# Kernel tuning notes

Hardware: AMD Instinct MI355X
Metric: run time of the kernel (lower is better)

## Reference

```python
import jax, jax.numpy as jnp
import numpy as np

E, L, M, F, S, P = 4, 10, 512, 128, 1000, 10  # envs, labels, max_sample, features, sample_size, batch_len


def setup_inputs() -> dict:
    key = jax.random.key(0)
    k1, k2, k3 = jax.random.split(key, 3)
    data_len = jax.random.randint(k1, (E, L), M // 2, M + 1, dtype=jnp.int32)
    matrix = jax.random.normal(k2, (E, L, M, F), dtype=jnp.float32)
    # zero out padded samples beyond data_len (as shape_to_matrix does)
    pad_mask = jnp.arange(M)[None, None, :, None] < data_len[:, :, None, None]
    matrix = matrix * pad_mask
    params = jnp.eye(F, dtype=jnp.float32) + 0.01 * jax.random.normal(k3, (F, F), dtype=jnp.float32)
    is_train_env = jnp.array([True, True, False, False])
    return {"matrix": matrix, "params": params, "data_len": data_len, "is_train_env": is_train_env}


def reference(matrix, params, data_len, is_train_env):
    lenf = data_len.astype(matrix.dtype)  # [E,L], torch keeps this as float32
    # __init__ preprocessing: normalize by mean std over sample dim (detached in torch)
    std = jax.lax.stop_gradient(jnp.std(matrix, axis=2).mean())
    mat = matrix / std
    # Silverman-style bandwidth on the normalized matrix (detached in torch)
    bw = jax.lax.stop_gradient(1.06 * (M ** (-1.0 / 5.0)) * jnp.std(mat, axis=2).mean())
    offset = jnp.exp(-0.5 / bw ** 2)
    proj = jnp.einsum('elmf,fg->elmg', mat, params)  # [E,L,M,F]
    left = jax.lax.stop_gradient(proj.min())   # .item() in torch -> constant
    right = jax.lax.stop_gradient(proj.max())
    delta = (right - left) / S
    x_grid = jnp.linspace(left, right, S)
    divisor = jnp.sqrt(2.0 * jnp.pi) * bw

    def step(acc, points):  # points: [P] grid chunk
        d2 = (proj[..., None] - points) ** 2                     # [E,L,M,F,P]
        s = jnp.sum(offset ** d2, axis=2)                        # [E,L,F,P]
        # remove contribution of zero-padded samples, then normalize by true count
        corr = (M - lenf)[:, :, None] * (offset ** (points ** 2))[None, None, :]  # [E,L,P]
        r = (s - corr[:, :, None, :]) / lenf[:, :, None, None]   # [E,L,F,P]
        d = jnp.sum(jnp.abs(r[:, None] - r[None, :]), axis=-1)   # [E,E,L,F] pairwise L1 over grid chunk
        return acc + d, None

    store_dis, _ = jax.lax.scan(step, jnp.zeros((E, E, L, F), proj.dtype), x_grid.reshape(S // P, P))
    store_dis = store_dis / divisor  # [E,E,L,F]

    idx = jnp.arange(E)
    upper = idx[:, None] < idx[None, :]                                   # all env pairs i<j
    train_pair = upper & is_train_env[:, None] & is_train_env[None, :]    # train env pairs i<j
    half = store_dis * (delta / 2.0)
    neg = jnp.array(-jnp.inf, half.dtype)
    test_results = jnp.where(upper[:, :, None, None], half, neg).max(axis=(0, 1))        # [L,F]
    train_results = jnp.where(train_pair[:, :, None, None], half, neg).max(axis=(0, 1))  # [L,F]
    train_dis = train_results.max(axis=0).mean()
    test_dis = test_results.max(axis=0).mean()
    return train_results, test_results, train_dis, test_dis
```

## Files before the change

### kernel.cpp

```cpp
#include <hip/hip_runtime.h>
#include <cmath>

#define E_ 4
#define L_ 10
#define M_ 512
#define F_ 128
#define S_ 1000

typedef unsigned int u32;
typedef _Float16 f16;
typedef __attribute__((ext_vector_type(8))) _Float16 v8h;
typedef __attribute__((ext_vector_type(4))) float v4f;

__device__ __forceinline__ float fexp2(float a){
#if __has_builtin(__builtin_amdgcn_exp2f)
  return __builtin_amdgcn_exp2f(a);
#else
  return exp2f(a);
#endif
}


__global__ __launch_bounds__(256) void k_pre(const float* __restrict__ mat,
                       const float* __restrict__ par,
                       float* __restrict__ projT, float* __restrict__ wsf){
  __shared__ float sm[2048];
  int b = blockIdx.x, tid = threadIdx.x;
  if (b >= 1280){
    int el = b - 1280;
    int fq = (tid & 31) * 4, part = tid >> 5;
    const float* base = mat + ((size_t)el * M_ + part*64) * F_;
    float4 s  = make_float4(0.f,0.f,0.f,0.f);
    float4 s2 = make_float4(0.f,0.f,0.f,0.f);
    #pragma unroll 8
    for (int i = 0; i < 64; i++){
      float4 v = *(const float4*)&base[i*F_ + fq];
      s.x += v.x; s.y += v.y; s.z += v.z; s.w += v.w;
      s2.x += v.x*v.x; s2.y += v.y*v.y; s2.z += v.z*v.z; s2.w += v.w*v.w;
    }
    ((float4*)sm)[tid]       = s;
    ((float4*)sm)[256 + tid] = s2;
    __syncthreads();
    for (int g = 4; g >= 1; g >>= 1){
      if (part < g){
        float4 o  = ((float4*)sm)[tid + g*32];
        float4 o2 = ((float4*)sm)[256 + tid + g*32];
        s.x += o.x; s.y += o.y; s.z += o.z; s.w += o.w;
        s2.x += o2.x; s2.y += o2.y; s2.z += o2.z; s2.w += o2.w;
        ((float4*)sm)[tid] = s;
        ((float4*)sm)[256 + tid] = s2;
      }
      __syncthreads();
    }
    if (part == 0){
      *(float4*)&wsf[2576 + el*128 + fq] = s;
      *(float4*)&wsf[7696 + el*128 + fq] = s2;
    }
    return;
  }
  int el = b >> 5, mt = (b & 31) * 16;
  int lane = tid & 63, wave = tid >> 6;
  int q = (lane >> 4) & 3, m16 = lane & 15;
  const float* arow = mat + ((size_t)el * M_ + mt + m16) * F_;
  v4f acc0 = {0.f,0.f,0.f,0.f}, acc1 = {0.f,0.f,0.f,0.f};
  #pragma unroll
  for (int c = 0; c < 4; c++){
    float4 a0 = *(const float4*)&arow[c*32 + q*8];
    float4 a1 = *(const float4*)&arow[c*32 + q*8 + 4];
    v8h af, b0, b1;
    af[0]=(f16)a0.x; af[1]=(f16)a0.y; af[2]=(f16)a0.z; af[3]=(f16)a0.w;
    af[4]=(f16)a1.x; af[5]=(f16)a1.y; af[6]=(f16)a1.z; af[7]=(f16)a1.w;
    const float* pb = par + (c*32 + q*8)*F_ + wave*32 + m16;
    #pragma unroll
    for (int j = 0; j < 8; j++){
      b0[j] = (f16)pb[j*F_];
      b1[j] = (f16)pb[j*F_ + 16];
    }
    acc0 = __builtin_amdgcn_mfma_f32_16x16x32_f16(af, b0, acc0, 0, 0, 0);
    acc1 = __builtin_amdgcn_mfma_f32_16x16x32_f16(af, b1, acc1, 0, 0, 0);
  }
  *(float4*)(projT + ((size_t)el*F_ + wave*32      + m16)*M_ + mt + q*4)
      = make_float4(acc0[0], acc0[1], acc0[2], acc0[3]);
  *(float4*)(projT + ((size_t)el*F_ + wave*32 + 16 + m16)*M_ + mt + q*4)
      = make_float4(acc1[0], acc1[1], acc1[2], acc1[3]);
  float lmin =  3.4e38f, lmax = -3.4e38f;
  #pragma unroll
  for (int r = 0; r < 4; r++){
    lmin = fminf(lmin, fminf(acc0[r], acc1[r]));
    lmax = fmaxf(lmax, fmaxf(acc0[r], acc1[r]));
  }
  #pragma unroll
  for (int d = 32; d >= 1; d >>= 1){
    lmin = fminf(lmin, __shfl_xor(lmin, d, 64));
    lmax = fmaxf(lmax, __shfl_xor(lmax, d, 64));
  }
  if (lane == 0){ sm[wave] = lmin; sm[8+wave] = lmax; }
  __syncthreads();
  if (tid == 0){
    wsf[16   + b] = fminf(fminf(sm[0], sm[1]), fminf(sm[2], sm[3]));
    wsf[1296 + b] = fmaxf(fmaxf(sm[8], sm[9]), fmaxf(sm[10], sm[11]));
  }
}

__global__ __launch_bounds__(1024) void k_red(float* __restrict__ wsf,
                                              float divisor, float k2c){
  __shared__ float rmn[1024], rmx[1024], rs[1024];
  int tid = threadIdx.x;
  float mn = 3.4e38f, mx = -3.4e38f, s = 0.f;
  for (int i = tid; i < 1280; i += 1024){
    mn = fminf(mn, wsf[16   + i]);
    mx = fmaxf(mx, wsf[1296 + i]);
  }
  for (int i = tid; i < 5120; i += 1024){
    float a  = wsf[2576 + i];
    float a2 = wsf[7696 + i];
    float mean = a * (1.0f/512.0f);
    float var  = a2 * (1.0f/512.0f) - mean*mean;
    s += sqrtf(fmaxf(var, 0.0f));
  }
  rmn[tid] = mn; rmx[tid] = mx; rs[tid] = s;
  __syncthreads();
  for (int g = 512; g >= 1; g >>= 1){
    if (tid < g){
      rmn[tid] = fminf(rmn[tid], rmn[tid+g]);
      rmx[tid] = fmaxf(rmx[tid], rmx[tid+g]);
      rs[tid] += rs[tid+g];
    }
    __syncthreads();
  }
  float rstd   = 5120.0f / rs[0];
  float leftS  = rmn[0] * rstd;
  float rightS = rmx[0] * rstd;
  float stepFS = (rightS - leftS) * (1.0f/999.0f);
  if (tid == 0){
    float inv2 = 1.0f / (2.0f * stepFS);
    wsf[0] = rstd * inv2;
    wsf[1] = leftS * inv2;
    wsf[2] = stepFS;
    wsf[3] = leftS;
    wsf[8] = ((rightS - leftS) * (1.0f/1000.0f)) * 0.5f / divisor;
  }
  float sh = 2.0f * stepFS;
  if (tid < 152){
    float v = 0.f;
    if (tid >= 8){
      int pr = (tid >> 1) - 4;
      int u  = pr - 34;
      float d = (tid & 1) ? (float)(2*u-1) * sh : (float)(2*u) * sh;
      v = (pr < 69) ? fexp2(k2c*d*d) : 0.f;
    }
    wsf[16 + tid] = v;
  }
  if (tid >= 256 && tid < 512){
    int idx = tid - 256;
    float xc = fmaf((float)(idx - 1), 4.0f*stepFS, leftS);
    wsf[168 + idx] = fexp2(k2c * xc * xc);
  }
}

__global__ __launch_bounds__(256, 4) void k_kde(const float* __restrict__ projT,
                      const int* __restrict__ dlen, const float* __restrict__ wsf,
                      float* __restrict__ dpair){
  __shared__ __align__(16) float smem[4752];
  int b = blockIdx.x;
  int l = b >> 7, f = b & 127;
  int tid = threadIdx.x, wave = tid >> 6, lane = tid & 63;
  int e = wave;
  const float4* gp = (const float4*)(projT + (((size_t)e * L_ + l) * F_ + f) * M_);
  float4 g0 = gp[lane], g1 = gp[lane + 64];
  float posScale = wsf[0], posOff = wsf[1];
  float lenE = (float)dlen[e*L_ + l];
  for (int idx = tid; idx < 824; idx += 256)
    ((float4*)(smem + 1024))[idx] = make_float4(0.f,0.f,0.f,0.f);
  if (tid < 38)
    ((float4*)(smem + 4320))[tid] = ((const float4*)(wsf + 16))[tid];
  if (tid >= 64 && tid < 128)
    ((float4*)(smem + 4472))[tid - 64] = ((const float4*)(wsf + 168))[tid - 64];
  __syncthreads();
  {
    float* hf = smem + 1024 + e*824;
    float pv[8] = {g0.x,g0.y,g0.z,g0.w,g1.x,g1.y,g1.z,g1.w};
    #pragma unroll
    for (int i = 0; i < 8; i++){
      float pos = fmaf(pv[i], posScale, -posOff);
      float n = floorf(pos + 0.5f);
      float d = pos - n;
      float wm = 0.5f*(0.5f-d)*(0.5f-d);
      float wp = 0.5f*(0.5f+d)*(0.5f+d);
      float w0 = 0.75f - d*d;
      int b0 = (int)n + 71;
      int b1 = b0 + 1, b2 = b0 + 2;
      int W0 = b0 + ((b0>>3)<<1);
      int W1 = b1 + ((b1>>3)<<1);
      int W2 = b2 + ((b2>>3)<<1);
      atomicAdd(&hf[W0], wm);
      atomicAdd(&hf[W1], w0);
      atomicAdd(&hf[W2], wp);
    }
  }
  __syncthreads();
  float rlen = 1.0f / lenE;
  float padc = 512.0f - lenE;
  {
    const float2* sK2 = (const float2*)(smem + 4320);
    const float* hl = smem + 1024 + e*824 + 10*lane;
    float2 c0 = sK2[72], c1 = sK2[73], c2 = sK2[74], c3 = sK2[75];
    float a0=0.f, a1=0.f, a2=0.f, a3=0.f;
    #pragma unroll 3
    for (int g = 0; g < 9; g++){
      float2 Hb[8];
      #pragma unroll
      for (int j = 0; j < 8; j++){
        int i = g*8 + j + 1;
        Hb[j] = *(const float2*)&hl[2*i + 2*(i>>2)];
      }
      #pragma unroll
      for (int j = 0; j < 8; j++){
        int i = g*8 + j + 1;
        a0 = fmaf(Hb[j].x, c0.x, fmaf(Hb[j].y, c0.y, a0));
        a1 = fmaf(Hb[j].x, c1.x, fmaf(Hb[j].y, c1.y, a1));
        a2 = fmaf(Hb[j].x, c2.x, fmaf(Hb[j].y, c2.y, a2));
        a3 = fmaf(Hb[j].x, c3.x, fmaf(Hb[j].y, c3.y, a3));
        c3 = c2; c2 = c1; c1 = c0; c0 = sK2[72 - i];
      }
    }
    int o0 = 4*lane;
    float4 cr = *(const float4*)&smem[4472 + o0];
    float4 stv = make_float4((a0 - padc*cr.x)*rlen, (a1 - padc*cr.y)*rlen,
                             (a2 - padc*cr.z)*rlen, (a3 - padc*cr.w)*rlen);
    *(float4*)&smem[e*256 + o0] = stv;
  }
  __syncthreads();
  float ps[6] = {0,0,0,0,0,0};
  if (tid < 250){
    float x[4][4];
    #pragma unroll
    for (int ee=0; ee<4; ee++){
      const float* st = &smem[ee*256 + tid];
      x[ee][0]=st[0]; x[ee][1]=st[1]; x[ee][2]=st[2]; x[ee][3]=st[3];
    }
    #pragma unroll
    for (int k=0; k<4; k++){
      float u = (float)k * 0.25f;
      float um1 = u - 1.0f, um2 = u - 2.0f, up1 = u + 1.0f;
      float w0 = -u * um1 * um2 * (1.0f/6.0f);
      float w1 = up1 * um1 * um2 * 0.5f;
      float w2 = -u * up1 * um2 * 0.5f;
      float w3 = u * up1 * um1 * (1.0f/6.0f);
      float rr[4];
      #pragma unroll
      for (int ee=0; ee<4; ee++)
        rr[ee] = w0*x[ee][0] + w1*x[ee][1] + w2*x[ee][2] + w3*x[ee][3];
      ps[0] += fabsf(rr[0]-rr[1]);
      ps[1] += fabsf(rr[0]-rr[2]);
      ps[2] += fabsf(rr[0]-rr[3]);
      ps[3] += fabsf(rr[1]-rr[2]);
      ps[4] += fabsf(rr[1]-rr[3]);
      ps[5] += fabsf(rr[2]-rr[3]);
    }
  }
  #pragma unroll
  for (int pr=0; pr<6; pr++){
    float v = ps[pr];
    #pragma unroll
    for (int d=32; d>=1; d>>=1) v += __shfl_xor(v, d, 64);
    if (lane == 0) smem[4728 + wave*6 + pr] = v;
  }
  __syncthreads();
  if (tid < 6)
    dpair[tid*1280 + b] = smem[4728+tid] + smem[4734+tid] + smem[4740+tid] + smem[4746+tid];
}

__global__ void k_fin(const float* __restrict__ dpair, const float* __restrict__ wsf,
                      const int* __restrict__ istrain, float* __restrict__ out){
  __shared__ float str[1280], ste[1280];
  __shared__ float s1[128], s2[128];
  int tid = threadIdx.x;
  float hscale = wsf[8];
  bool t0 = istrain[0]!=0, t1 = istrain[1]!=0, t2 = istrain[2]!=0, t3 = istrain[3]!=0;
  bool trn[6] = { t0&&t1, t0&&t2, t0&&t3, t1&&t2, t1&&t3, t2&&t3 };
  for (int idx = tid; idx < 1280; idx += 256){
    float tmax = -INFINITY, trmax = -INFINITY;
    #pragma unroll
    for (int pr=0;pr<6;pr++){
      float h = dpair[pr*1280 + idx] * hscale;
      tmax = fmaxf(tmax, h);
      if (trn[pr]) trmax = fmaxf(trmax, h);
    }
    out[idx]        = trmax;
    out[1280 + idx] = tmax;
    str[idx] = trmax; ste[idx] = tmax;
  }
  __syncthreads();
  if (tid < 128){
    float m1 = -INFINITY, m2 = -INFINITY;
    for (int l=0;l<L_;l++){
      m1 = fmaxf(m1, str[l*F_ + tid]);
      m2 = fmaxf(m2, ste[l*F_ + tid]);
    }
    s1[tid] = m1; s2[tid] = m2;
  }
  __syncthreads();
  for (int g=64; g>=1; g>>=1){
    if (tid < g){ s1[tid] += s1[tid+g]; s2[tid] += s2[tid+g]; }
    __syncthreads();
  }
  if (tid == 0){
    out[2560] = s1[0] * (1.0f/128.0f);
    out[2561] = s2[0] * (1.0f/128.0f);
  }
}

extern "C" void kernel_launch(void* const* d_in, const int* in_sizes, int n_in,
                              void* d_out, int out_size, void* d_ws, size_t ws_size,
                              hipStream_t stream){
  const float* mat = (const float*)d_in[0];
  const float* par = (const float*)d_in[1];
  const int*  dlen = (const int*)d_in[2];
  const int*  istr = (const int*)d_in[3];
  float* out   = (float*)d_out;
  float* wsf   = (float*)d_ws;
  float* dpair = wsf + 12816;
  float* projT = wsf + 20496;

  double bw_d   = 1.06 * pow(512.0, -0.2);
  float  bw     = (float)bw_d;
  float  offset = expf(-0.5f / (bw*bw));
  float  k2c    = (float)(log((double)offset) * 1.4426950408889634);
  float  divisor = sqrtf(6.283185307179586f) * bw;

  k_pre <<<1320, 256, 0, stream>>>(mat, par, projT, wsf);
  k_red <<<1,   1024, 0, stream>>>(wsf, divisor, k2c);
  k_kde <<<1280, 256, 0, stream>>>(projT, dlen, wsf, dpair);
  k_fin <<<1,    256, 0, stream>>>(dpair, wsf, istr, out);
}
```

Baseline: 142.9 us.

## Replace reduction kernel with global atomics and recompute grid constants per KDE block

```diff
diff --git a/kernel.cpp b/kernel.cpp
--- a/kernel.cpp
+++ b/kernel.cpp
@@ -20,12 +20,21 @@
 #endif
 }
 
+__device__ __forceinline__ u32 fkey(float x){
+  u32 b = __float_as_uint(x);
+  return (b & 0x80000000u) ? ~b : (b | 0x80000000u);
+}
+__device__ __forceinline__ float funkey(u32 k){
+  return __uint_as_float((k & 0x80000000u) ? (k & 0x7fffffffu) : ~k);
+}
+
 
 __global__ __launch_bounds__(256) void k_pre(const float* __restrict__ mat,
                        const float* __restrict__ par,
                        float* __restrict__ projT, float* __restrict__ wsf){
   __shared__ float sm[2048];
   int b = blockIdx.x, tid = threadIdx.x;
+  u32* wsu = (u32*)wsf;
   if (b >= 1280){
     int el = b - 1280;
     int fq = (tid & 31) * 4, part = tid >> 5;
@@ -53,8 +62,15 @@
       __syncthreads();
     }
     if (part == 0){
-      *(float4*)&wsf[2576 + el*128 + fq] = s;
-      *(float4*)&wsf[7696 + el*128 + fq] = s2;
+      const float r512 = 1.0f/512.0f;
+      float m0 = s.x*r512, m1 = s.y*r512, m2 = s.z*r512, m3 = s.w*r512;
+      float pss = sqrtf(fmaxf(s2.x*r512 - m0*m0, 0.0f))
+                + sqrtf(fmaxf(s2.y*r512 - m1*m1, 0.0f))
+                + sqrtf(fmaxf(s2.z*r512 - m2*m2, 0.0f))
+                + sqrtf(fmaxf(s2.w*r512 - m3*m3, 0.0f));
+      #pragma unroll
+      for (int d = 16; d >= 1; d >>= 1) pss += __shfl_xor(pss, d, 64);
+      if (tid == 0) atomicAdd(&wsf[6], pss);
     }
     return;
   }
@@ -97,49 +113,38 @@
   if (lane == 0){ sm[wave] = lmin; sm[8+wave] = lmax; }
   __syncthreads();
   if (tid == 0){
-    wsf[16   + b] = fminf(fminf(sm[0], sm[1]), fminf(sm[2], sm[3]));
-    wsf[1296 + b] = fmaxf(fmaxf(sm[8], sm[9]), fmaxf(sm[10], sm[11]));
-  }
-}
-
-__global__ __launch_bounds__(1024) void k_red(float* __restrict__ wsf,
-                                              float divisor, float k2c){
-  __shared__ float rmn[1024], rmx[1024], rs[1024];
-  int tid = threadIdx.x;
-  float mn = 3.4e38f, mx = -3.4e38f, s = 0.f;
-  for (int i = tid; i < 1280; i += 1024){
-    mn = fminf(mn, wsf[16   + i]);
-    mx = fmaxf(mx, wsf[1296 + i]);
-  }
-  for (int i = tid; i < 5120; i += 1024){
-    float a  = wsf[2576 + i];
-    float a2 = wsf[7696 + i];
-    float mean = a * (1.0f/512.0f);
-    float var  = a2 * (1.0f/512.0f) - mean*mean;
-    s += sqrtf(fmaxf(var, 0.0f));
-  }
-  rmn[tid] = mn; rmx[tid] = mx; rs[tid] = s;
-  __syncthreads();
-  for (int g = 512; g >= 1; g >>= 1){
-    if (tid < g){
-      rmn[tid] = fminf(rmn[tid], rmn[tid+g]);
-      rmx[tid] = fmaxf(rmx[tid], rmx[tid+g]);
-      rs[tid] += rs[tid+g];
-    }
-    __syncthreads();
-  }
-  float rstd   = 5120.0f / rs[0];
-  float leftS  = rmn[0] * rstd;
-  float rightS = rmx[0] * rstd;
+    float bmin = fminf(fminf(sm[0], sm[1]), fminf(sm[2], sm[3]));
+    float bmax = fmaxf(fmaxf(sm[8], sm[9]), fmaxf(sm[10], sm[11]));
+    atomicMax(&wsu[4], ~fkey(bmin));
+    atomicMax(&wsu[5],  fkey(bmax));
+  }
+}
+
+__global__ __launch_bounds__(256) void k_kde(const float* __restrict__ projT,
+                      const int* __restrict__ dlen, const float* __restrict__ wsf,
+                      float* __restrict__ dpair, float k2c){
+  __shared__ __align__(16) float smem[4752];
+  int b = blockIdx.x;
+  int l = b >> 7, f = b & 127;
+  int tid = threadIdx.x, wave = tid >> 6, lane = tid & 63;
+  int e = wave;
+  const float4* gp = (const float4*)(projT + (((size_t)e * L_ + l) * F_ + f) * M_);
+  float4 g0 = gp[lane], g1 = gp[lane + 64];
+  float lenE = (float)dlen[e*L_ + l];
+  const u32* wsu = (const u32*)wsf;
+  u32 kA = wsu[4], kB = wsu[5];
+  float ssum = wsf[6];
+  for (int idx = tid; idx < 824; idx += 256)
+    ((float4*)(smem + 1024))[idx] = make_float4(0.f,0.f,0.f,0.f);
+  float leftV  = funkey(~kA);
+  float rightV = funkey(kB);
+  float rstd   = 5120.0f / ssum;
+  float leftS  = leftV * rstd;
+  float rightS = rightV * rstd;
   float stepFS = (rightS - leftS) * (1.0f/999.0f);
-  if (tid == 0){
-    float inv2 = 1.0f / (2.0f * stepFS);
-    wsf[0] = rstd * inv2;
-    wsf[1] = leftS * inv2;
-    wsf[2] = stepFS;
-    wsf[3] = leftS;
-    wsf[8] = ((rightS - leftS) * (1.0f/1000.0f)) * 0.5f / divisor;
-  }
+  float inv2   = 1.0f / (2.0f * stepFS);
+  float posScale = rstd * inv2;
+  float posOff   = leftS * inv2;
   float sh = 2.0f * stepFS;
   if (tid < 152){
     float v = 0.f;
@@ -149,33 +154,12 @@
       float d = (tid & 1) ? (float)(2*u-1) * sh : (float)(2*u) * sh;
       v = (pr < 69) ? fexp2(k2c*d*d) : 0.f;
     }
-    wsf[16 + tid] = v;
-  }
-  if (tid >= 256 && tid < 512){
-    int idx = tid - 256;
-    float xc = fmaf((float)(idx - 1), 4.0f*stepFS, leftS);
-    wsf[168 + idx] = fexp2(k2c * xc * xc);
-  }
-}
-
-__global__ __launch_bounds__(256, 4) void k_kde(const float* __restrict__ projT,
-                      const int* __restrict__ dlen, const float* __restrict__ wsf,
-                      float* __restrict__ dpair){
-  __shared__ __align__(16) float smem[4752];
-  int b = blockIdx.x;
-  int l = b >> 7, f = b & 127;
-  int tid = threadIdx.x, wave = tid >> 6, lane = tid & 63;
-  int e = wave;
-  const float4* gp = (const float4*)(projT + (((size_t)e * L_ + l) * F_ + f) * M_);
-  float4 g0 = gp[lane], g1 = gp[lane + 64];
-  float posScale = wsf[0], posOff = wsf[1];
-  float lenE = (float)dlen[e*L_ + l];
-  for (int idx = tid; idx < 824; idx += 256)
-    ((float4*)(smem + 1024))[idx] = make_float4(0.f,0.f,0.f,0.f);
-  if (tid < 38)
-    ((float4*)(smem + 4320))[tid] = ((const float4*)(wsf + 16))[tid];
-  if (tid >= 64 && tid < 128)
-    ((float4*)(smem + 4472))[tid - 64] = ((const float4*)(wsf + 168))[tid - 64];
+    smem[4320 + tid] = v;
+  }
+  {
+    float xc = fmaf((float)(tid - 1), 4.0f*stepFS, leftS);
+    smem[4472 + tid] = fexp2(k2c * xc * xc);
+  }
   __syncthreads();
   {
     float* hf = smem + 1024 + e*824;
@@ -202,11 +186,13 @@
   float rlen = 1.0f / lenE;
   float padc = 512.0f - lenE;
   {
-    const float2* sK2 = (const float2*)(smem + 4320);
+    const float4* sK4 = (const float4*)(smem + 4320);
     const float* hl = smem + 1024 + e*824 + 10*lane;
-    float2 c0 = sK2[72], c1 = sK2[73], c2 = sK2[74], c3 = sK2[75];
+    float4 i0 = sK4[36], i1 = sK4[37];
+    float2 c0 = make_float2(i0.x,i0.y), c1 = make_float2(i0.z,i0.w);
+    float2 c2 = make_float2(i1.x,i1.y), c3 = make_float2(i1.z,i1.w);
     float a0=0.f, a1=0.f, a2=0.f, a3=0.f;
-    #pragma unroll 3
+    #pragma unroll
     for (int g = 0; g < 9; g++){
       float2 Hb[8];
       #pragma unroll
@@ -214,14 +200,19 @@
         int i = g*8 + j + 1;
         Hb[j] = *(const float2*)&hl[2*i + 2*(i>>2)];
       }
+      float4 t3 = sK4[35-4*g], t2_ = sK4[34-4*g];
+      float4 t1_ = sK4[33-4*g], t0_ = sK4[32-4*g];
+      float2 nc[8] = { make_float2(t3.z,t3.w),  make_float2(t3.x,t3.y),
+                       make_float2(t2_.z,t2_.w), make_float2(t2_.x,t2_.y),
+                       make_float2(t1_.z,t1_.w), make_float2(t1_.x,t1_.y),
+                       make_float2(t0_.z,t0_.w), make_float2(t0_.x,t0_.y) };
       #pragma unroll
       for (int j = 0; j < 8; j++){
-        int i = g*8 + j + 1;
         a0 = fmaf(Hb[j].x, c0.x, fmaf(Hb[j].y, c0.y, a0));
         a1 = fmaf(Hb[j].x, c1.x, fmaf(Hb[j].y, c1.y, a1));
         a2 = fmaf(Hb[j].x, c2.x, fmaf(Hb[j].y, c2.y, a2));
         a3 = fmaf(Hb[j].x, c3.x, fmaf(Hb[j].y, c3.y, a3));
-        c3 = c2; c2 = c1; c1 = c0; c0 = sK2[72 - i];
+        c3 = c2; c2 = c1; c1 = c0; c0 = nc[j];
       }
     }
     int o0 = 4*lane;
@@ -272,11 +263,16 @@
 }
 
 __global__ void k_fin(const float* __restrict__ dpair, const float* __restrict__ wsf,
-                      const int* __restrict__ istrain, float* __restrict__ out){
+                      const int* __restrict__ istrain, float* __restrict__ out,
+                      float divisor){
   __shared__ float str[1280], ste[1280];
   __shared__ float s1[128], s2[128];
   int tid = threadIdx.x;
-  float hscale = wsf[8];
+  const u32* wsu = (const u32*)wsf;
+  float leftV  = funkey(~wsu[4]);
+  float rightV = funkey(wsu[5]);
+  float rstd   = 5120.0f / wsf[6];
+  float hscale = ((rightV - leftV) * rstd * (1.0f/1000.0f)) * 0.5f / divisor;
   bool t0 = istrain[0]!=0, t1 = istrain[1]!=0, t2 = istrain[2]!=0, t3 = istrain[3]!=0;
   bool trn[6] = { t0&&t1, t0&&t2, t0&&t3, t1&&t2, t1&&t3, t2&&t3 };
   for (int idx = tid; idx < 1280; idx += 256){
@@ -329,8 +325,8 @@
   float  k2c    = (float)(log((double)offset) * 1.4426950408889634);
   float  divisor = sqrtf(6.283185307179586f) * bw;
 
+  hipMemsetAsync(wsf + 4, 0, 12, stream);
   k_pre <<<1320, 256, 0, stream>>>(mat, par, projT, wsf);
-  k_red <<<1,   1024, 0, stream>>>(wsf, divisor, k2c);
-  k_kde <<<1280, 256, 0, stream>>>(projT, dlen, wsf, dpair);
-  k_fin <<<1,    256, 0, stream>>>(dpair, wsf, istr, out);
-}
+  k_kde <<<1280, 256, 0, stream>>>(projT, dlen, wsf, dpair, k2c);
+  k_fin <<<1,    256, 0, stream>>>(dpair, wsf, istr, out, divisor);
+}
```

Result: slower. 162.8 us (+13.9%).
